# Kernel tuning notes

Measured on AMD Instinct MI355X. Metric: run time of the kernel, lower is better.

The kernel has to match this reference:

```python
import jax, jax.numpy as jnp
import numpy as np

N_NODES = 50000   # batch_size * num_nodes
N_EDGES = 800000
D_IN = 128
D_OUT = 128


def setup_inputs() -> dict:
    key = jax.random.key(0)
    k1, k2, k3, k4 = jax.random.split(key, 4)
    x = jax.random.normal(k1, (N_NODES, D_IN), dtype=jnp.float32)
    edge_index = jax.random.randint(k2, (2, N_EDGES), 0, N_NODES, dtype=jnp.int64)
    W = jax.random.normal(k3, (D_OUT, D_IN), dtype=jnp.float32) * (1.0 / np.sqrt(D_IN))
    b = jax.random.normal(k4, (D_OUT,), dtype=jnp.float32) * 0.01
    return {"x": x, "edge_index": edge_index, "batch_size": 50, "num_nodes": 1000, "W": W, "b": b}


def reference(x, edge_index, batch_size, num_nodes, W, b):
    dim_size = batch_size * num_nodes
    row, col = edge_index[0], edge_index[1]
    # gather messages and segment-mean aggregate over destination rows
    msgs = x[col]                                   # [E, D_IN]
    summed = jax.ops.segment_sum(msgs, row, num_segments=dim_size)      # [N, D_IN]
    counts = jax.ops.segment_sum(jnp.ones((row.shape[0],), dtype=x.dtype), row,
                                 num_segments=dim_size)                 # [N]
    mean = summed / jnp.maximum(counts, 1.0)[:, None]                   # 0 for empty rows
    # linear projection (torch Linear: y = x @ W.T + b)
    return mean @ W.T + b
```

## Files before the change

### kernel.cpp

```cpp
#include <hip/hip_runtime.h>

#define D 128
#define BSHIFT 6
#define BCAP 1536
#define EPB_A 2048

typedef unsigned short ushort_t;
typedef unsigned int uint_t;
typedef __attribute__((ext_vector_type(8))) short short8_t;
typedef __attribute__((ext_vector_type(4))) float f32x4_t;

__device__ __forceinline__ bool eidx_is64(const int* eidx) {
    int lane = threadIdx.x & 63;
    int probe = eidx[2 * lane + 1];
    return __ballot(probe != 0) == 0ULL;
}

__device__ __forceinline__ uint_t f2bf(float f) {
    union { float f; uint_t i; } v; v.f = f;
    return (v.i + 0x7fffu + ((v.i >> 16) & 1u)) >> 16;
}
__device__ __forceinline__ float bf_lo(uint_t w) {
    union { uint_t i; float f; } v; v.i = w << 16; return v.f;
}
__device__ __forceinline__ float bf_hi(uint_t w) {
    union { uint_t i; float f; } v; v.i = w & 0xffff0000u; return v.f;
}

__global__ __launch_bounds__(256) void pre_kernel(
    const int* __restrict__ eidx, int* __restrict__ gcur,
    int* __restrict__ bucket, int E, int NBUK, int ab,
    const float* __restrict__ x, uint_t* __restrict__ xb, int total8, int cvb,
    const float* __restrict__ Wsrc, uint_t* __restrict__ wb, int N) {
    int t = threadIdx.x;

    if ((int)blockIdx.x >= ab) {
        if (xb == nullptr) return;
        int cb = blockIdx.x - ab;
        if (cb < cvb) {
            int i = cb * 256 + t;
            if (i < total8) {
                const float4* p = (const float4*)(x + (size_t)i * 8);
                float4 a = p[0], b = p[1];
                uint4 o;
                o.x = f2bf(a.x) | (f2bf(a.y) << 16);
                o.y = f2bf(a.z) | (f2bf(a.w) << 16);
                o.z = f2bf(b.x) | (f2bf(b.y) << 16);
                o.w = f2bf(b.z) | (f2bf(b.w) << 16);
                *(uint4*)(xb + (size_t)i * 4) = o;
            }
            if (cb == 0 && t < 16) {
                uint4 z; z.x = 0u; z.y = 0u; z.z = 0u; z.w = 0u;
                ((uint4*)(xb + (size_t)N * (D / 2)))[t] = z;
            }
        } else {
            int i = (cb - cvb) * 256 + t;
            if (i < D * D / 8) {
                const float4* p = (const float4*)(Wsrc + (size_t)i * 8);
                float4 a = p[0], b = p[1];
                uint4 o;
                o.x = f2bf(a.x) | (f2bf(a.y) << 16);
                o.y = f2bf(a.z) | (f2bf(a.w) << 16);
                o.z = f2bf(b.x) | (f2bf(b.y) << 16);
                o.w = f2bf(b.z) | (f2bf(b.w) << 16);
                *(uint4*)(wb + (size_t)i * 4) = o;
            }
        }
        return;
    }

    __shared__ int lhist[1024];
    __shared__ int lbase[1024];
    bool is64 = eidx_is64(eidx);
    for (int i = t; i < NBUK; i += 256) lhist[i] = 0;
    __syncthreads();

    int e0 = blockIdx.x * EPB_A;
    int e1 = min(e0 + EPB_A, E);
    int rr[8], cc[8];
    #pragma unroll
    for (int k = 0; k < 8; ++k) {
        int e = e0 + t + k * 256;
        rr[k] = -1;
        if (e < e1) {
            if (is64) { rr[k] = eidx[2 * e]; cc[k] = eidx[2 * E + 2 * e]; }
            else      { rr[k] = eidx[e];     cc[k] = eidx[E + e]; }
            atomicAdd(&lhist[rr[k] >> BSHIFT], 1);
        }
    }
    __syncthreads();
    for (int i = t; i < NBUK; i += 256) {
        int h = lhist[i];
        lbase[i] = (h > 0) ? atomicAdd(&gcur[i], h) : 0;
        lhist[i] = 0;
    }
    __syncthreads();
    #pragma unroll
    for (int k = 0; k < 8; ++k) {
        if (rr[k] >= 0) {
            int b = rr[k] >> BSHIFT;
            int p = atomicAdd(&lhist[b], 1);
            int idx = lbase[b] + p;
            if (idx < BCAP) bucket[b * BCAP + idx] = ((rr[k] & 63) << 24) | cc[k];
        }
    }
}

#define GATHER8(CA, CB)                                                       \
    {                                                                         \
        uint4 g0 = *(const uint4*)(xs + (size_t)(CA).x * D);                  \
        uint4 g1 = *(const uint4*)(xs + (size_t)(CA).y * D);                  \
        uint4 g2 = *(const uint4*)(xs + (size_t)(CA).z * D);                  \
        uint4 g3 = *(const uint4*)(xs + (size_t)(CA).w * D);                  \
        uint4 g4 = *(const uint4*)(xs + (size_t)(CB).x * D);                  \
        uint4 g5 = *(const uint4*)(xs + (size_t)(CB).y * D);                  \
        uint4 g6 = *(const uint4*)(xs + (size_t)(CB).z * D);                  \
        uint4 g7 = *(const uint4*)(xs + (size_t)(CB).w * D);                  \
        a0 += ((bf_lo(g0.x) + bf_lo(g1.x)) + (bf_lo(g2.x) + bf_lo(g3.x)))     \
            + ((bf_lo(g4.x) + bf_lo(g5.x)) + (bf_lo(g6.x) + bf_lo(g7.x)));    \
        a1 += ((bf_hi(g0.x) + bf_hi(g1.x)) + (bf_hi(g2.x) + bf_hi(g3.x)))     \
            + ((bf_hi(g4.x) + bf_hi(g5.x)) + (bf_hi(g6.x) + bf_hi(g7.x)));    \
        a2 += ((bf_lo(g0.y) + bf_lo(g1.y)) + (bf_lo(g2.y) + bf_lo(g3.y)))     \
            + ((bf_lo(g4.y) + bf_lo(g5.y)) + (bf_lo(g6.y) + bf_lo(g7.y)));    \
        a3 += ((bf_hi(g0.y) + bf_hi(g1.y)) + (bf_hi(g2.y) + bf_hi(g3.y)))     \
            + ((bf_hi(g4.y) + bf_hi(g5.y)) + (bf_hi(g6.y) + bf_hi(g7.y)));    \
        a4 += ((bf_lo(g0.z) + bf_lo(g1.z)) + (bf_lo(g2.z) + bf_lo(g3.z)))     \
            + ((bf_lo(g4.z) + bf_lo(g5.z)) + (bf_lo(g6.z) + bf_lo(g7.z)));    \
        a5 += ((bf_hi(g0.z) + bf_hi(g1.z)) + (bf_hi(g2.z) + bf_hi(g3.z)))     \
            + ((bf_hi(g4.z) + bf_hi(g5.z)) + (bf_hi(g6.z) + bf_hi(g7.z)));    \
        a6 += ((bf_lo(g0.w) + bf_lo(g1.w)) + (bf_lo(g2.w) + bf_lo(g3.w)))     \
            + ((bf_lo(g4.w) + bf_lo(g5.w)) + (bf_lo(g6.w) + bf_lo(g7.w)));    \
        a7 += ((bf_hi(g0.w) + bf_hi(g1.w)) + (bf_hi(g2.w) + bf_hi(g3.w)))     \
            + ((bf_hi(g4.w) + bf_hi(g5.w)) + (bf_hi(g6.w) + bf_hi(g7.w)));    \
    }

#define GATHER16(CA, CB, CC, CD)                                              \
    {                                                                         \
        uint4 g0 = *(const uint4*)(xs + (size_t)(CA).x * D);                  \
        uint4 g1 = *(const uint4*)(xs + (size_t)(CA).y * D);                  \
        uint4 g2 = *(const uint4*)(xs + (size_t)(CA).z * D);                  \
        uint4 g3 = *(const uint4*)(xs + (size_t)(CA).w * D);                  \
        uint4 g4 = *(const uint4*)(xs + (size_t)(CB).x * D);                  \
        uint4 g5 = *(const uint4*)(xs + (size_t)(CB).y * D);                  \
        uint4 g6 = *(const uint4*)(xs + (size_t)(CB).z * D);                  \
        uint4 g7 = *(const uint4*)(xs + (size_t)(CB).w * D);                  \
        uint4 g8 = *(const uint4*)(xs + (size_t)(CC).x * D);                  \
        uint4 g9 = *(const uint4*)(xs + (size_t)(CC).y * D);                  \
        uint4 ga = *(const uint4*)(xs + (size_t)(CC).z * D);                  \
        uint4 gb = *(const uint4*)(xs + (size_t)(CC).w * D);                  \
        uint4 gc = *(const uint4*)(xs + (size_t)(CD).x * D);                  \
        uint4 gd = *(const uint4*)(xs + (size_t)(CD).y * D);                  \
        uint4 ge = *(const uint4*)(xs + (size_t)(CD).z * D);                  \
        uint4 gf = *(const uint4*)(xs + (size_t)(CD).w * D);                  \
        a0 += (((bf_lo(g0.x) + bf_lo(g1.x)) + (bf_lo(g2.x) + bf_lo(g3.x)))    \
             + ((bf_lo(g4.x) + bf_lo(g5.x)) + (bf_lo(g6.x) + bf_lo(g7.x))))   \
            + (((bf_lo(g8.x) + bf_lo(g9.x)) + (bf_lo(ga.x) + bf_lo(gb.x)))    \
             + ((bf_lo(gc.x) + bf_lo(gd.x)) + (bf_lo(ge.x) + bf_lo(gf.x))));  \
        a1 += (((bf_hi(g0.x) + bf_hi(g1.x)) + (bf_hi(g2.x) + bf_hi(g3.x)))    \
             + ((bf_hi(g4.x) + bf_hi(g5.x)) + (bf_hi(g6.x) + bf_hi(g7.x))))   \
            + (((bf_hi(g8.x) + bf_hi(g9.x)) + (bf_hi(ga.x) + bf_hi(gb.x)))    \
             + ((bf_hi(gc.x) + bf_hi(gd.x)) + (bf_hi(ge.x) + bf_hi(gf.x))));  \
        a2 += (((bf_lo(g0.y) + bf_lo(g1.y)) + (bf_lo(g2.y) + bf_lo(g3.y)))    \
             + ((bf_lo(g4.y) + bf_lo(g5.y)) + (bf_lo(g6.y) + bf_lo(g7.y))))   \
            + (((bf_lo(g8.y) + bf_lo(g9.y)) + (bf_lo(ga.y) + bf_lo(gb.y)))    \
             + ((bf_lo(gc.y) + bf_lo(gd.y)) + (bf_lo(ge.y) + bf_lo(gf.y))));  \
        a3 += (((bf_hi(g0.y) + bf_hi(g1.y)) + (bf_hi(g2.y) + bf_hi(g3.y)))    \
             + ((bf_hi(g4.y) + bf_hi(g5.y)) + (bf_hi(g6.y) + bf_hi(g7.y))))   \
            + (((bf_hi(g8.y) + bf_hi(g9.y)) + (bf_hi(ga.y) + bf_hi(gb.y)))    \
             + ((bf_hi(gc.y) + bf_hi(gd.y)) + (bf_hi(ge.y) + bf_hi(gf.y))));  \
        a4 += (((bf_lo(g0.z) + bf_lo(g1.z)) + (bf_lo(g2.z) + bf_lo(g3.z)))    \
             + ((bf_lo(g4.z) + bf_lo(g5.z)) + (bf_lo(g6.z) + bf_lo(g7.z))))   \
            + (((bf_lo(g8.z) + bf_lo(g9.z)) + (bf_lo(ga.z) + bf_lo(gb.z)))    \
             + ((bf_lo(gc.z) + bf_lo(gd.z)) + (bf_lo(ge.z) + bf_lo(gf.z))));  \
        a5 += (((bf_hi(g0.z) + bf_hi(g1.z)) + (bf_hi(g2.z) + bf_hi(g3.z)))    \
             + ((bf_hi(g4.z) + bf_hi(g5.z)) + (bf_hi(g6.z) + bf_hi(g7.z))))   \
            + (((bf_hi(g8.z) + bf_hi(g9.z)) + (bf_hi(ga.z) + bf_hi(gb.z)))    \
             + ((bf_hi(gc.z) + bf_hi(gd.z)) + (bf_hi(ge.z) + bf_hi(gf.z))));  \
        a6 += (((bf_lo(g0.w) + bf_lo(g1.w)) + (bf_lo(g2.w) + bf_lo(g3.w)))    \
             + ((bf_lo(g4.w) + bf_lo(g5.w)) + (bf_lo(g6.w) + bf_lo(g7.w))))   \
            + (((bf_lo(g8.w) + bf_lo(g9.w)) + (bf_lo(ga.w) + bf_lo(gb.w)))    \
             + ((bf_lo(gc.w) + bf_lo(gd.w)) + (bf_lo(ge.w) + bf_lo(gf.w))));  \
        a7 += (((bf_hi(g0.w) + bf_hi(g1.w)) + (bf_hi(g2.w) + bf_hi(g3.w)))    \
             + ((bf_hi(g4.w) + bf_hi(g5.w)) + (bf_hi(g6.w) + bf_hi(g7.w))))   \
            + (((bf_hi(g8.w) + bf_hi(g9.w)) + (bf_hi(ga.w) + bf_hi(gb.w)))    \
             + ((bf_hi(gc.w) + bf_hi(gd.w)) + (bf_hi(ge.w) + bf_hi(gf.w))));  \
    }

__global__ __launch_bounds__(512, 2) void fused_bf_kernel(
    const ushort_t* __restrict__ xb, const int* __restrict__ gcur,
    const int* __restrict__ bucket, const ushort_t* __restrict__ Wb,
    const float* __restrict__ bias, float* __restrict__ out, int N) {
    __shared__ int sE[2048];
    __shared__ int lcnt[64], lpos[64], lstart[64];
    __shared__ ushort_t sA[64 * 136];
    int t = threadIdx.x;
    int b = blockIdx.x;

    if (t < 64) { lcnt[t] = 0; lpos[t] = 0; }
    __syncthreads();
    int tot = min(gcur[b], BCAP);
    const int* bp = bucket + (size_t)b * BCAP;
    for (int i = t; i < tot; i += 512)
        atomicAdd(&lcnt[bp[i] >> 24], 1);
    __syncthreads();
    if (t == 0) {
        int run = 0;
        #pragma unroll
        for (int i = 0; i < 64; ++i) {
            lstart[i] = run;
            run += (lcnt[i] + 7) & ~7;
        }
    }
    __syncthreads();
    for (int i = t; i < tot; i += 512) {
        int v = bp[i];
        int rl = v >> 24;
        int p = atomicAdd(&lpos[rl], 1);
        int idx = lstart[rl] + p;
        if (idx < 2048) sE[idx] = v & 0xFFFFFF;
    }
    if (t < 64) {
        int c0 = lcnt[t];
        int pe = (c0 + 7) & ~7;
        for (int p = c0; p < pe; ++p) {
            int idx = lstart[t] + p;
            if (idx < 2048) sE[idx] = N;
        }
    }
    __syncthreads();

    int lane = t & 63, wave = t >> 6;
    int qi = t >> 4, sl = t & 15;
    int nbase = b << BSHIFT;
    const ushort_t* xs = xb + 8 * sl;

    #pragma unroll
    for (int quad = 0; quad < 2; ++quad) {
        int n = 2 * qi + quad;
        int nr  = lcnt[n];
        int st  = lstart[n];
        int nr8 = (nr + 7) & ~7;
        float a0 = 0.f, a1 = 0.f, a2 = 0.f, a3 = 0.f;
        float a4 = 0.f, a5 = 0.f, a6 = 0.f, a7 = 0.f;
        int i = 0;
        for (; i + 16 <= nr8; i += 16) {
            int4 cA = *(const int4*)(sE + st + i);
            int4 cB = *(const int4*)(sE + st + i + 4);
            int4 cC = *(const int4*)(sE + st + i + 8);
            int4 cD = *(const int4*)(sE + st + i + 12);
            GATHER16(cA, cB, cC, cD)
        }
        if (i + 8 <= nr8) {
            int4 dA = *(const int4*)(sE + st + i);
            int4 dB = *(const int4*)(sE + st + i + 4);
            GATHER8(dA, dB)
        }
        float inv = (nr > 0) ? 1.0f / (float)nr : 0.0f;
        uint4 pk;
        pk.x = f2bf(a0 * inv) | (f2bf(a1 * inv) << 16);
        pk.y = f2bf(a2 * inv) | (f2bf(a3 * inv) << 16);
        pk.z = f2bf(a4 * inv) | (f2bf(a5 * inv) << 16);
        pk.w = f2bf(a6 * inv) | (f2bf(a7 * inv) << 16);
        *(uint4*)(sA + n * 136 + 8 * sl) = pk;
    }
    __syncthreads();

    {
        int rt = wave & 3, jgrp = wave >> 2;
        int ml = lane & 15, kh = lane >> 4;
        short8_t afr[4];
        #pragma unroll
        for (int ks = 0; ks < 4; ++ks)
            afr[ks] = *(const short8_t*)(sA + (rt * 16 + ml) * 136 + ks * 32 + kh * 8);
        f32x4_t acc[4];
        #pragma unroll
        for (int q = 0; q < 4; ++q) acc[q] = (f32x4_t){0.f, 0.f, 0.f, 0.f};
        #pragma unroll
        for (int q = 0; q < 4; ++q) {
            int j = (jgrp * 4 + q) * 16 + ml;
            #pragma unroll
            for (int ks = 0; ks < 4; ++ks) {
                short8_t bfr = *(const short8_t*)(Wb + (size_t)j * D + ks * 32 + kh * 8);
                acc[q] = __builtin_amdgcn_mfma_f32_16x16x32_bf16(afr[ks], bfr, acc[q], 0, 0, 0);
            }
        }
        #pragma unroll
        for (int q = 0; q < 4; ++q) {
            int j = (jgrp * 4 + q) * 16 + ml;
            float bj = bias[j];
            #pragma unroll
            for (int r = 0; r < 4; ++r) {
                int gn = nbase + rt * 16 + kh * 4 + r;
                if (gn < N) out[(size_t)gn * D + j] = acc[q][r] + bj;
            }
        }
    }
}

__global__ __launch_bounds__(256) void prep_kernel(
    const int* __restrict__ gcur, const int* __restrict__ bucket,
    int* __restrict__ elist, int* __restrict__ cnt,
    int* __restrict__ start, int N, int NBUK) {
    __shared__ int lcnt[64], lpos[64], lstart[64];
    int t = threadIdx.x;
    int b = blockIdx.x;
    if (t < 64) { lcnt[t] = 0; lpos[t] = 0; }
    __syncthreads();
    int tot = min(gcur[b], BCAP);
    const int* bp = bucket + (size_t)b * BCAP;
    for (int i = t; i < tot; i += 256)
        atomicAdd(&lcnt[bp[i] >> 24], 1);
    __syncthreads();
    if (t == 0) {
        int run = 0;
        #pragma unroll
        for (int i = 0; i < 64; ++i) {
            lstart[i] = run;
            run += (lcnt[i] + 3) & ~3;
        }
    }
    __syncthreads();
    for (int i = t; i < tot; i += 256) {
        int v = bp[i];
        int rl = v >> 24;
        int p = atomicAdd(&lpos[rl], 1);
        int idx = lstart[rl] + p;
        if (idx < BCAP) elist[(size_t)b * BCAP + idx] = v & 0xFFFFFF;
    }
    if (t < 64) {
        int gr = (b << BSHIFT) + t;
        if (gr < N) { cnt[gr] = lcnt[t]; start[gr] = b * BCAP + lstart[t]; }
    }
}

__global__ __launch_bounds__(256, 6) void fused_kernel(
    const float* __restrict__ x, const int* __restrict__ elist,
    const int* __restrict__ cnt, const int* __restrict__ start,
    const float* __restrict__ W, const float* __restrict__ bias,
    float* __restrict__ out, int N) {
    __shared__ float sT[128 * 36];
    __shared__ float wc[16 * 132];
    int t = threadIdx.x;
    int lane = t & 63, wave = t >> 6;
    int half = lane >> 5, sl = lane & 31;
    int nbase = blockIdx.x * 32;

    #pragma unroll
    for (int pair = 0; pair < 4; ++pair) {
        int n = wave * 8 + pair * 2 + half;
        int gn = nbase + n;
        int nr  = (gn < N) ? cnt[gn]   : 0;
        int beg = (gn < N) ? start[gn] : 0;
        int nro  = __shfl(nr, lane ^ 32);
        int both = min(nr, nro);
        float ax = 0.f, ay = 0.f, az = 0.f, aw = 0.f;
        int i = 0;
        for (; i + 8 <= both; i += 8) {
            int4 cA = *(const int4*)(elist + beg + i);
            int4 cB = *(const int4*)(elist + beg + i + 4);
            float4 v0 = *(const float4*)(x + (size_t)cA.x * D + 4 * sl);
            float4 v1 = *(const float4*)(x + (size_t)cA.y * D + 4 * sl);
            float4 v2 = *(const float4*)(x + (size_t)cA.z * D + 4 * sl);
            float4 v3 = *(const float4*)(x + (size_t)cA.w * D + 4 * sl);
            float4 v4 = *(const float4*)(x + (size_t)cB.x * D + 4 * sl);
            float4 v5 = *(const float4*)(x + (size_t)cB.y * D + 4 * sl);
            float4 v6 = *(const float4*)(x + (size_t)cB.z * D + 4 * sl);
            float4 v7 = *(const float4*)(x + (size_t)cB.w * D + 4 * sl);
            ax += ((v0.x + v1.x) + (v2.x + v3.x)) + ((v4.x + v5.x) + (v6.x + v7.x));
            ay += ((v0.y + v1.y) + (v2.y + v3.y)) + ((v4.y + v5.y) + (v6.y + v7.y));
            az += ((v0.z + v1.z) + (v2.z + v3.z)) + ((v4.z + v5.z) + (v6.z + v7.z));
            aw += ((v0.w + v1.w) + (v2.w + v3.w)) + ((v4.w + v5.w) + (v6.w + v7.w));
        }
        for (; i < nr; ++i) {
            int c0 = elist[beg + i];
            float4 v = *(const float4*)(x + (size_t)c0 * D + 4 * sl);
            ax += v.x; ay += v.y; az += v.z; aw += v.w;
        }
        float inv = (nr > 0) ? 1.0f / (float)nr : 0.0f;
        int k0 = 4 * sl;
        sT[(k0 + 0) * 36 + n] = ax * inv;
        sT[(k0 + 1) * 36 + n] = ay * inv;
        sT[(k0 + 2) * 36 + n] = az * inv;
        sT[(k0 + 3) * 36 + n] = aw * inv;
    }

    int jg = t & 31, ng = t >> 5;
    int j0 = jg * 4, n0 = ng * 4;
    float acc[4][4] = {};
    for (int kc = 0; kc < 8; ++kc) {
        __syncthreads();
        #pragma unroll
        for (int i = 0; i < 8; ++i) {
            int idx = t + i * 256;
            int j = idx >> 4, kk = idx & 15;
            wc[kk * 132 + j] = W[j * D + kc * 16 + kk];
        }
        __syncthreads();
        #pragma unroll
        for (int kk = 0; kk < 16; ++kk) {
            int k = kc * 16 + kk;
            float4 s4 = *(const float4*)(sT + k * 36 + n0);
            float4 w4 = *(const float4*)(wc + kk * 132 + j0);
            acc[0][0] = fmaf(s4.x, w4.x, acc[0][0]); acc[0][1] = fmaf(s4.x, w4.y, acc[0][1]);
            acc[0][2] = fmaf(s4.x, w4.z, acc[0][2]); acc[0][3] = fmaf(s4.x, w4.w, acc[0][3]);
            acc[1][0] = fmaf(s4.y, w4.x, acc[1][0]); acc[1][1] = fmaf(s4.y, w4.y, acc[1][1]);
            acc[1][2] = fmaf(s4.y, w4.z, acc[1][2]); acc[1][3] = fmaf(s4.y, w4.w, acc[1][3]);
            acc[2][0] = fmaf(s4.z, w4.x, acc[2][0]); acc[2][1] = fmaf(s4.z, w4.y, acc[2][1]);
            acc[2][2] = fmaf(s4.z, w4.z, acc[2][2]); acc[2][3] = fmaf(s4.z, w4.w, acc[2][3]);
            acc[3][0] = fmaf(s4.w, w4.x, acc[3][0]); acc[3][1] = fmaf(s4.w, w4.y, acc[3][1]);
            acc[3][2] = fmaf(s4.w, w4.z, acc[3][2]); acc[3][3] = fmaf(s4.w, w4.w, acc[3][3]);
        }
    }
    float4 b4 = *(const float4*)(bias + j0);
    #pragma unroll
    for (int i = 0; i < 4; ++i) {
        int gn = nbase + n0 + i;
        if (gn >= N) continue;
        float4 o;
        o.x = acc[i][0] + b4.x;
        o.y = acc[i][1] + b4.y;
        o.z = acc[i][2] + b4.z;
        o.w = acc[i][3] + b4.w;
        *(float4*)(out + (size_t)gn * D + j0) = o;
    }
}

__global__ __launch_bounds__(256) void scatter_kernel(
    const float* __restrict__ x, const int* __restrict__ eidx,
    float* summed, float* __restrict__ counts, int E) {
    int t = blockIdx.x * 256 + threadIdx.x;
    int lane = threadIdx.x & 63;
    bool is64 = eidx_is64(eidx);
    int e = t >> 6;
    if (e >= E) return;
    int d = lane * 2;
    int r, c;
    if (is64) { r = eidx[2 * e]; c = eidx[2 * E + 2 * e]; }
    else      { r = eidx[e];     c = eidx[E + e]; }
    float2 v = *(const float2*)(x + (size_t)c * D + d);
    float* dst = summed + (size_t)r * D + d;
    atomicAdd(dst, v.x);
    atomicAdd(dst + 1, v.y);
    if (lane == 0) atomicAdd(counts + r, 1.0f);
}

__global__ __launch_bounds__(256) void divide_kernel(
    float* __restrict__ sums, const float* __restrict__ counts, int N) {
    int g = blockIdx.x * 256 + threadIdx.x;
    int r = g >> 6, lane = g & 63;
    if (r >= N) return;
    float inv = 1.0f / fmaxf(counts[r], 1.0f);
    float2* p = (float2*)(sums + (size_t)r * D + 2 * lane);
    float2 v = *p;
    v.x *= inv; v.y *= inv;
    *p = v;
}

__global__ __launch_bounds__(256) void gemm_kernel(
    float* inout, const float* __restrict__ W,
    const float* __restrict__ bias, int N) {
    __shared__ float sT[128 * 36];
    __shared__ float wc[32 * 132];
    int t = threadIdx.x;
    int nbase = blockIdx.x * 32;
    #pragma unroll
    for (int i = 0; i < 16; ++i) {
        int idx = t + i * 256;
        int n = idx >> 7, k = idx & 127;
        int gn = nbase + n;
        sT[k * 36 + n] = (gn < N) ? inout[(size_t)gn * D + k] : 0.0f;
    }
    int jg = t & 31, ng = t >> 5;
    int j0 = jg * 4, n0 = ng * 4;
    float acc[4][4] = {};
    for (int kc = 0; kc < 4; ++kc) {
        __syncthreads();
        #pragma unroll
        for (int i = 0; i < 16; ++i) {
            int idx = t + i * 256;
            int j = idx >> 5, kk = idx & 31;
            wc[kk * 132 + j] = W[j * D + kc * 32 + kk];
        }
        __syncthreads();
        #pragma unroll 8
        for (int kk = 0; kk < 32; ++kk) {
            int k = kc * 32 + kk;
            float4 s4 = *(const float4*)(sT + k * 36 + n0);
            float4 w4 = *(const float4*)(wc + kk * 132 + j0);
            acc[0][0] = fmaf(s4.x, w4.x, acc[0][0]); acc[0][1] = fmaf(s4.x, w4.y, acc[0][1]);
            acc[0][2] = fmaf(s4.x, w4.z, acc[0][2]); acc[0][3] = fmaf(s4.x, w4.w, acc[0][3]);
            acc[1][0] = fmaf(s4.y, w4.x, acc[1][0]); acc[1][1] = fmaf(s4.y, w4.y, acc[1][1]);
            acc[1][2] = fmaf(s4.y, w4.z, acc[1][2]); acc[1][3] = fmaf(s4.y, w4.w, acc[1][3]);
            acc[2][0] = fmaf(s4.z, w4.x, acc[2][0]); acc[2][1] = fmaf(s4.z, w4.y, acc[2][1]);
            acc[2][2] = fmaf(s4.z, w4.z, acc[2][2]); acc[2][3] = fmaf(s4.z, w4.w, acc[2][3]);
            acc[3][0] = fmaf(s4.w, w4.x, acc[3][0]); acc[3][1] = fmaf(s4.w, w4.y, acc[3][1]);
            acc[3][2] = fmaf(s4.w, w4.z, acc[3][2]); acc[3][3] = fmaf(s4.w, w4.w, acc[3][3]);
        }
    }
    float4 b4 = *(const float4*)(bias + j0);
    #pragma unroll
    for (int i = 0; i < 4; ++i) {
        int gn = nbase + n0 + i;
        if (gn >= N) continue;
        float4 o;
        o.x = acc[i][0] + b4.x;
        o.y = acc[i][1] + b4.y;
        o.z = acc[i][2] + b4.z;
        o.w = acc[i][3] + b4.w;
        *(float4*)(inout + (size_t)gn * D + j0) = o;
    }
}

extern "C" void kernel_launch(void* const* d_in, const int* in_sizes, int n_in,
                              void* d_out, int out_size, void* d_ws, size_t ws_size,
                              hipStream_t stream) {
    const float* x = (const float*)d_in[0];
    const int* eidx = (const int*)d_in[1];
    const float* W = (const float*)d_in[4];
    const float* b = (const float*)d_in[5];
    float* out = (float*)d_out;

    int N = in_sizes[0] / D;
    int E = in_sizes[1] / 2;
    int NBUK = (N + 63) >> BSHIFT;
    int ab = (E + EPB_A - 1) / EPB_A;

    size_t o0 = 0;
    size_t o_gc = o0;  o0 += ((size_t)NBUK * 4 + 255) & ~255ULL;
    size_t o_cn = o0;  o0 += ((size_t)N * 4 + 255) & ~255ULL;
    size_t o_st = o0;  o0 += ((size_t)N * 4 + 255) & ~255ULL;
    size_t o_bk = o0;  o0 += (size_t)NBUK * BCAP * 4;
    size_t o_el = o0;  o0 += (size_t)NBUK * BCAP * 4;
    size_t base_need = o0;
    size_t o_xb = o0;  o0 += (((size_t)(N + 1) * D * 2) + 255) & ~255ULL;
    size_t o_wb = o0;  size_t bf_need = o0 + (size_t)D * D * 2;

    bool cap_ok = (N <= 65536) && ((size_t)NBUK * BCAP >= (size_t)E);

    int cvb = (N * D / 8 + 255) / 256;
    int wvb = (D * D / 8 + 255) / 256;

    if (cap_ok && ws_size >= bf_need) {
        char* ws = (char*)d_ws;
        int*      gcur  = (int*)(ws + o_gc);
        int*      bkt   = (int*)(ws + o_bk);
        ushort_t* xb    = (ushort_t*)(ws + o_xb);
        ushort_t* wb    = (ushort_t*)(ws + o_wb);

        hipMemsetAsync(gcur, 0, (size_t)NBUK * 4, stream);
        pre_kernel<<<ab + cvb + wvb, 256, 0, stream>>>(
            eidx, gcur, bkt, E, NBUK, ab,
            x, (uint_t*)xb, N * D / 8, cvb, W, (uint_t*)wb, N);
        fused_bf_kernel<<<NBUK, 512, 0, stream>>>(xb, gcur, bkt, wb, b, out, N);
    } else if (cap_ok && ws_size >= base_need) {
        char* ws = (char*)d_ws;
        int* gcur  = (int*)(ws + o_gc);
        int* cnt   = (int*)(ws + o_cn);
        int* start = (int*)(ws + o_st);
        int* bkt   = (int*)(ws + o_bk);
        int* elist = (int*)(ws + o_el);
        int fb = (N + 31) / 32;

        hipMemsetAsync(gcur, 0, (size_t)NBUK * 4, stream);
        pre_kernel<<<ab, 256, 0, stream>>>(
            eidx, gcur, bkt, E, NBUK, ab,
            nullptr, nullptr, 0, 0, nullptr, nullptr, N);
        prep_kernel<<<NBUK, 256, 0, stream>>>(gcur, bkt, elist, cnt, start, N, NBUK);
        fused_kernel<<<fb, 256, 0, stream>>>(x, elist, cnt, start, W, b, out, N);
    } else {
        float* counts = (float*)d_ws;
        int fb = (N + 31) / 32;
        hipMemsetAsync(d_out, 0, (size_t)N * D * sizeof(float), stream);
        hipMemsetAsync(d_ws, 0, (size_t)N * sizeof(float), stream);
        int sb = (E * 64 + 255) / 256;
        scatter_kernel<<<sb, 256, 0, stream>>>(x, eidx, out, counts, E);
        int db = (N * 64 + 255) / 256;
        divide_kernel<<<db, 256, 0, stream>>>(out, counts, N);
        gemm_kernel<<<fb, 256, 0, stream>>>(out, W, b, N);
    }
}
```

Before: 156.9 us.

## Double-buffer neighbor gathers via global_load_lds and shrink buckets to 32 rows

The bf16 gather now uses direct global-to-LDS async loads (global_load_lds) into a per-wave double-buffered staging area, issuing the next four rows before accumulating the current ones, in place of register-based 8/16-wide gathers. Buckets shrink from 64 to 32 destination rows (BCAP 1024), and the fused kernel drops to 256 threads per block, so there are twice as many smaller blocks. The aim is to overlap gather latency with accumulation and raise block-level parallelism. In exchange, each thread has fewer loads in flight, there are more waitcnt stalls, LDS use per block is larger, and the smaller bucket capacity gives less headroom before edges are dropped.

```diff
diff --git a/kernel.cpp b/kernel.cpp
--- a/kernel.cpp
+++ b/kernel.cpp
@@ -1,14 +1,16 @@
 #include <hip/hip_runtime.h>
 
 #define D 128
-#define BSHIFT 6
-#define BCAP 1536
+#define BSHIFT 5
+#define BCAP 1024
 #define EPB_A 2048
 
 typedef unsigned short ushort_t;
 typedef unsigned int uint_t;
 typedef __attribute__((ext_vector_type(8))) short short8_t;
 typedef __attribute__((ext_vector_type(4))) float f32x4_t;
+typedef const __attribute__((address_space(1))) void* gas_cptr;
+typedef __attribute__((address_space(3))) void* las_ptr;
 
 __device__ __forceinline__ bool eidx_is64(const int* eidx) {
     int lane = threadIdx.x & 63;
@@ -69,8 +71,8 @@
         return;
     }
 
-    __shared__ int lhist[1024];
-    __shared__ int lbase[1024];
+    __shared__ int lhist[2048];
+    __shared__ int lbase[2048];
     bool is64 = eidx_is64(eidx);
     for (int i = t; i < NBUK; i += 256) lhist[i] = 0;
     __syncthreads();
@@ -101,130 +103,74 @@
             int b = rr[k] >> BSHIFT;
             int p = atomicAdd(&lhist[b], 1);
             int idx = lbase[b] + p;
-            if (idx < BCAP) bucket[b * BCAP + idx] = ((rr[k] & 63) << 24) | cc[k];
-        }
-    }
-}
-
-#define GATHER8(CA, CB)                                                       \
+            if (idx < BCAP) bucket[b * BCAP + idx] = ((rr[k] & 31) << 24) | cc[k];
+        }
+    }
+}
+
+#define ISSUE(c, bufsel)                                                      \
     {                                                                         \
-        uint4 g0 = *(const uint4*)(xs + (size_t)(CA).x * D);                  \
-        uint4 g1 = *(const uint4*)(xs + (size_t)(CA).y * D);                  \
-        uint4 g2 = *(const uint4*)(xs + (size_t)(CA).z * D);                  \
-        uint4 g3 = *(const uint4*)(xs + (size_t)(CA).w * D);                  \
-        uint4 g4 = *(const uint4*)(xs + (size_t)(CB).x * D);                  \
-        uint4 g5 = *(const uint4*)(xs + (size_t)(CB).y * D);                  \
-        uint4 g6 = *(const uint4*)(xs + (size_t)(CB).z * D);                  \
-        uint4 g7 = *(const uint4*)(xs + (size_t)(CB).w * D);                  \
-        a0 += ((bf_lo(g0.x) + bf_lo(g1.x)) + (bf_lo(g2.x) + bf_lo(g3.x)))     \
-            + ((bf_lo(g4.x) + bf_lo(g5.x)) + (bf_lo(g6.x) + bf_lo(g7.x)));    \
-        a1 += ((bf_hi(g0.x) + bf_hi(g1.x)) + (bf_hi(g2.x) + bf_hi(g3.x)))     \
-            + ((bf_hi(g4.x) + bf_hi(g5.x)) + (bf_hi(g6.x) + bf_hi(g7.x)));    \
-        a2 += ((bf_lo(g0.y) + bf_lo(g1.y)) + (bf_lo(g2.y) + bf_lo(g3.y)))     \
-            + ((bf_lo(g4.y) + bf_lo(g5.y)) + (bf_lo(g6.y) + bf_lo(g7.y)));    \
-        a3 += ((bf_hi(g0.y) + bf_hi(g1.y)) + (bf_hi(g2.y) + bf_hi(g3.y)))     \
-            + ((bf_hi(g4.y) + bf_hi(g5.y)) + (bf_hi(g6.y) + bf_hi(g7.y)));    \
-        a4 += ((bf_lo(g0.z) + bf_lo(g1.z)) + (bf_lo(g2.z) + bf_lo(g3.z)))     \
-            + ((bf_lo(g4.z) + bf_lo(g5.z)) + (bf_lo(g6.z) + bf_lo(g7.z)));    \
-        a5 += ((bf_hi(g0.z) + bf_hi(g1.z)) + (bf_hi(g2.z) + bf_hi(g3.z)))     \
-            + ((bf_hi(g4.z) + bf_hi(g5.z)) + (bf_hi(g6.z) + bf_hi(g7.z)));    \
-        a6 += ((bf_lo(g0.w) + bf_lo(g1.w)) + (bf_lo(g2.w) + bf_lo(g3.w)))     \
-            + ((bf_lo(g4.w) + bf_lo(g5.w)) + (bf_lo(g6.w) + bf_lo(g7.w)));    \
-        a7 += ((bf_hi(g0.w) + bf_hi(g1.w)) + (bf_hi(g2.w) + bf_hi(g3.w)))     \
-            + ((bf_hi(g4.w) + bf_hi(g5.w)) + (bf_hi(g6.w) + bf_hi(g7.w)));    \
-    }
-
-#define GATHER16(CA, CB, CC, CD)                                              \
-    {                                                                         \
-        uint4 g0 = *(const uint4*)(xs + (size_t)(CA).x * D);                  \
-        uint4 g1 = *(const uint4*)(xs + (size_t)(CA).y * D);                  \
-        uint4 g2 = *(const uint4*)(xs + (size_t)(CA).z * D);                  \
-        uint4 g3 = *(const uint4*)(xs + (size_t)(CA).w * D);                  \
-        uint4 g4 = *(const uint4*)(xs + (size_t)(CB).x * D);                  \
-        uint4 g5 = *(const uint4*)(xs + (size_t)(CB).y * D);                  \
-        uint4 g6 = *(const uint4*)(xs + (size_t)(CB).z * D);                  \
-        uint4 g7 = *(const uint4*)(xs + (size_t)(CB).w * D);                  \
-        uint4 g8 = *(const uint4*)(xs + (size_t)(CC).x * D);                  \
-        uint4 g9 = *(const uint4*)(xs + (size_t)(CC).y * D);                  \
-        uint4 ga = *(const uint4*)(xs + (size_t)(CC).z * D);                  \
-        uint4 gb = *(const uint4*)(xs + (size_t)(CC).w * D);                  \
-        uint4 gc = *(const uint4*)(xs + (size_t)(CD).x * D);                  \
-        uint4 gd = *(const uint4*)(xs + (size_t)(CD).y * D);                  \
-        uint4 ge = *(const uint4*)(xs + (size_t)(CD).z * D);                  \
-        uint4 gf = *(const uint4*)(xs + (size_t)(CD).w * D);                  \
-        a0 += (((bf_lo(g0.x) + bf_lo(g1.x)) + (bf_lo(g2.x) + bf_lo(g3.x)))    \
-             + ((bf_lo(g4.x) + bf_lo(g5.x)) + (bf_lo(g6.x) + bf_lo(g7.x))))   \
-            + (((bf_lo(g8.x) + bf_lo(g9.x)) + (bf_lo(ga.x) + bf_lo(gb.x)))    \
-             + ((bf_lo(gc.x) + bf_lo(gd.x)) + (bf_lo(ge.x) + bf_lo(gf.x))));  \
-        a1 += (((bf_hi(g0.x) + bf_hi(g1.x)) + (bf_hi(g2.x) + bf_hi(g3.x)))    \
-             + ((bf_hi(g4.x) + bf_hi(g5.x)) + (bf_hi(g6.x) + bf_hi(g7.x))))   \
-            + (((bf_hi(g8.x) + bf_hi(g9.x)) + (bf_hi(ga.x) + bf_hi(gb.x)))    \
-             + ((bf_hi(gc.x) + bf_hi(gd.x)) + (bf_hi(ge.x) + bf_hi(gf.x))));  \
-        a2 += (((bf_lo(g0.y) + bf_lo(g1.y)) + (bf_lo(g2.y) + bf_lo(g3.y)))    \
-             + ((bf_lo(g4.y) + bf_lo(g5.y)) + (bf_lo(g6.y) + bf_lo(g7.y))))   \
-            + (((bf_lo(g8.y) + bf_lo(g9.y)) + (bf_lo(ga.y) + bf_lo(gb.y)))    \
-             + ((bf_lo(gc.y) + bf_lo(gd.y)) + (bf_lo(ge.y) + bf_lo(gf.y))));  \
-        a3 += (((bf_hi(g0.y) + bf_hi(g1.y)) + (bf_hi(g2.y) + bf_hi(g3.y)))    \
-             + ((bf_hi(g4.y) + bf_hi(g5.y)) + (bf_hi(g6.y) + bf_hi(g7.y))))   \
-            + (((bf_hi(g8.y) + bf_hi(g9.y)) + (bf_hi(ga.y) + bf_hi(gb.y)))    \
-             + ((bf_hi(gc.y) + bf_hi(gd.y)) + (bf_hi(ge.y) + bf_hi(gf.y))));  \
-        a4 += (((bf_lo(g0.z) + bf_lo(g1.z)) + (bf_lo(g2.z) + bf_lo(g3.z)))    \
-             + ((bf_lo(g4.z) + bf_lo(g5.z)) + (bf_lo(g6.z) + bf_lo(g7.z))))   \
-            + (((bf_lo(g8.z) + bf_lo(g9.z)) + (bf_lo(ga.z) + bf_lo(gb.z)))    \
-             + ((bf_lo(gc.z) + bf_lo(gd.z)) + (bf_lo(ge.z) + bf_lo(gf.z))));  \
-        a5 += (((bf_hi(g0.z) + bf_hi(g1.z)) + (bf_hi(g2.z) + bf_hi(g3.z)))    \
-             + ((bf_hi(g4.z) + bf_hi(g5.z)) + (bf_hi(g6.z) + bf_hi(g7.z))))   \
-            + (((bf_hi(g8.z) + bf_hi(g9.z)) + (bf_hi(ga.z) + bf_hi(gb.z)))    \
-             + ((bf_hi(gc.z) + bf_hi(gd.z)) + (bf_hi(ge.z) + bf_hi(gf.z))));  \
-        a6 += (((bf_lo(g0.w) + bf_lo(g1.w)) + (bf_lo(g2.w) + bf_lo(g3.w)))    \
-             + ((bf_lo(g4.w) + bf_lo(g5.w)) + (bf_lo(g6.w) + bf_lo(g7.w))))   \
-            + (((bf_lo(g8.w) + bf_lo(g9.w)) + (bf_lo(ga.w) + bf_lo(gb.w)))    \
-             + ((bf_lo(gc.w) + bf_lo(gd.w)) + (bf_lo(ge.w) + bf_lo(gf.w))));  \
-        a7 += (((bf_hi(g0.w) + bf_hi(g1.w)) + (bf_hi(g2.w) + bf_hi(g3.w)))    \
-             + ((bf_hi(g4.w) + bf_hi(g5.w)) + (bf_hi(g6.w) + bf_hi(g7.w))))   \
-            + (((bf_hi(g8.w) + bf_hi(g9.w)) + (bf_hi(ga.w) + bf_hi(gb.w)))    \
-             + ((bf_hi(gc.w) + bf_hi(gd.w)) + (bf_hi(ge.w) + bf_hi(gf.w))));  \
-    }
-
-__global__ __launch_bounds__(512, 2) void fused_bf_kernel(
+        ushort_t* db_ = wstage + (bufsel) * 2048;                             \
+        __builtin_amdgcn_global_load_lds(                                     \
+            (gas_cptr)(xb + (size_t)(c).x * D + 8 * sl),                      \
+            (las_ptr)(db_), 16, 0, 0);                                        \
+        __builtin_amdgcn_global_load_lds(                                     \
+            (gas_cptr)(xb + (size_t)(c).y * D + 8 * sl),                      \
+            (las_ptr)(db_ + 512), 16, 0, 0);                                  \
+        __builtin_amdgcn_global_load_lds(                                     \
+            (gas_cptr)(xb + (size_t)(c).z * D + 8 * sl),                      \
+            (las_ptr)(db_ + 1024), 16, 0, 0);                                 \
+        __builtin_amdgcn_global_load_lds(                                     \
+            (gas_cptr)(xb + (size_t)(c).w * D + 8 * sl),                      \
+            (las_ptr)(db_ + 1536), 16, 0, 0);                                 \
+    }
+
+#define ACC(v)                                                                \
+    a0 += bf_lo((v).x); a1 += bf_hi((v).x);                                   \
+    a2 += bf_lo((v).y); a3 += bf_hi((v).y);                                   \
+    a4 += bf_lo((v).z); a5 += bf_hi((v).z);                                   \
+    a6 += bf_lo((v).w); a7 += bf_hi((v).w);
+
+__global__ __launch_bounds__(256, 3) void fused_bf_kernel(
     const ushort_t* __restrict__ xb, const int* __restrict__ gcur,
     const int* __restrict__ bucket, const ushort_t* __restrict__ Wb,
     const float* __restrict__ bias, float* __restrict__ out, int N) {
-    __shared__ int sE[2048];
-    __shared__ int lcnt[64], lpos[64], lstart[64];
-    __shared__ ushort_t sA[64 * 136];
+    __shared__ int sE[1024];
+    __shared__ int lcnt[32], lpos[32], lstart[32];
+    __shared__ ushort_t sA[32 * 136];
+    __shared__ ushort_t stage[16384];
     int t = threadIdx.x;
     int b = blockIdx.x;
 
-    if (t < 64) { lcnt[t] = 0; lpos[t] = 0; }
+    if (t < 32) { lcnt[t] = 0; lpos[t] = 0; }
     __syncthreads();
     int tot = min(gcur[b], BCAP);
     const int* bp = bucket + (size_t)b * BCAP;
-    for (int i = t; i < tot; i += 512)
+    for (int i = t; i < tot; i += 256)
         atomicAdd(&lcnt[bp[i] >> 24], 1);
     __syncthreads();
     if (t == 0) {
         int run = 0;
         #pragma unroll
-        for (int i = 0; i < 64; ++i) {
+        for (int i = 0; i < 32; ++i) {
             lstart[i] = run;
             run += (lcnt[i] + 7) & ~7;
         }
     }
     __syncthreads();
-    for (int i = t; i < tot; i += 512) {
+    for (int i = t; i < tot; i += 256) {
         int v = bp[i];
         int rl = v >> 24;
         int p = atomicAdd(&lpos[rl], 1);
         int idx = lstart[rl] + p;
-        if (idx < 2048) sE[idx] = v & 0xFFFFFF;
-    }
-    if (t < 64) {
+        if (idx < 1024) sE[idx] = v & 0xFFFFFF;
+    }
+    if (t < 32) {
         int c0 = lcnt[t];
         int pe = (c0 + 7) & ~7;
         for (int p = c0; p < pe; ++p) {
             int idx = lstart[t] + p;
-            if (idx < 2048) sE[idx] = N;
+            if (idx < 1024) sE[idx] = N;
         }
     }
     __syncthreads();
@@ -232,28 +178,42 @@
     int lane = t & 63, wave = t >> 6;
     int qi = t >> 4, sl = t & 15;
     int nbase = b << BSHIFT;
-    const ushort_t* xs = xb + 8 * sl;
+    ushort_t* wstage = stage + (wave << 12);
 
     #pragma unroll
     for (int quad = 0; quad < 2; ++quad) {
         int n = 2 * qi + quad;
-        int nr  = lcnt[n];
-        int st  = lstart[n];
-        int nr8 = (nr + 7) & ~7;
+        int nr = lcnt[n];
+        int st = lstart[n];
+        int trips = ((nr + 7) & ~7) >> 2;
+        int wmax = trips;
+        wmax = max(wmax, __shfl_xor(wmax, 16));
+        wmax = max(wmax, __shfl_xor(wmax, 32));
         float a0 = 0.f, a1 = 0.f, a2 = 0.f, a3 = 0.f;
         float a4 = 0.f, a5 = 0.f, a6 = 0.f, a7 = 0.f;
-        int i = 0;
-        for (; i + 16 <= nr8; i += 16) {
-            int4 cA = *(const int4*)(sE + st + i);
-            int4 cB = *(const int4*)(sE + st + i + 4);
-            int4 cC = *(const int4*)(sE + st + i + 8);
-            int4 cD = *(const int4*)(sE + st + i + 12);
-            GATHER16(cA, cB, cC, cD)
-        }
-        if (i + 8 <= nr8) {
-            int4 dA = *(const int4*)(sE + st + i);
-            int4 dB = *(const int4*)(sE + st + i + 4);
-            GATHER8(dA, dB)
+        if (wmax > 0) {
+            int4 c0 = (0 < trips) ? *(const int4*)(sE + st)
+                                  : make_int4(N, N, N, N);
+            ISSUE(c0, 0)
+            for (int bt = 0; bt < wmax; ++bt) {
+                int buf = bt & 1;
+                if (bt + 1 < wmax) {
+                    int4 cn = (bt + 1 < trips)
+                        ? *(const int4*)(sE + st + 4 * (bt + 1))
+                        : make_int4(N, N, N, N);
+                    ISSUE(cn, buf ^ 1)
+                    asm volatile("s_waitcnt vmcnt(4)" ::: "memory");
+                } else {
+                    asm volatile("s_waitcnt vmcnt(0)" ::: "memory");
+                }
+                __builtin_amdgcn_sched_barrier(0);
+                const ushort_t* sb = wstage + buf * 2048;
+                uint4 v0 = *(const uint4*)(sb +    0 + lane * 8);
+                uint4 v1 = *(const uint4*)(sb +  512 + lane * 8);
+                uint4 v2 = *(const uint4*)(sb + 1024 + lane * 8);
+                uint4 v3 = *(const uint4*)(sb + 1536 + lane * 8);
+                ACC(v0) ACC(v1) ACC(v2) ACC(v3)
+            }
         }
         float inv = (nr > 0) ? 1.0f / (float)nr : 0.0f;
         uint4 pk;
@@ -266,7 +226,7 @@
     __syncthreads();
 
     {
-        int rt = wave & 3, jgrp = wave >> 2;
+        int rt = wave & 1, jgrp = wave >> 1;
         int ml = lane & 15, kh = lane >> 4;
         short8_t afr[4];
         #pragma unroll
@@ -301,10 +261,10 @@
     const int* __restrict__ gcur, const int* __restrict__ bucket,
     int* __restrict__ elist, int* __restrict__ cnt,
     int* __restrict__ start, int N, int NBUK) {
-    __shared__ int lcnt[64], lpos[64], lstart[64];
+    __shared__ int lcnt[32], lpos[32], lstart[32];
     int t = threadIdx.x;
     int b = blockIdx.x;
-    if (t < 64) { lcnt[t] = 0; lpos[t] = 0; }
+    if (t < 32) { lcnt[t] = 0; lpos[t] = 0; }
     __syncthreads();
     int tot = min(gcur[b], BCAP);
     const int* bp = bucket + (size_t)b * BCAP;
@@ -314,7 +274,7 @@
     if (t == 0) {
         int run = 0;
         #pragma unroll
-        for (int i = 0; i < 64; ++i) {
+        for (int i = 0; i < 32; ++i) {
             lstart[i] = run;
             run += (lcnt[i] + 3) & ~3;
         }
@@ -327,7 +287,7 @@
         int idx = lstart[rl] + p;
         if (idx < BCAP) elist[(size_t)b * BCAP + idx] = v & 0xFFFFFF;
     }
-    if (t < 64) {
+    if (t < 32) {
         int gr = (b << BSHIFT) + t;
         if (gr < N) { cnt[gr] = lcnt[t]; start[gr] = b * BCAP + lstart[t]; }
     }
@@ -522,7 +482,7 @@
 
     int N = in_sizes[0] / D;
     int E = in_sizes[1] / 2;
-    int NBUK = (N + 63) >> BSHIFT;
+    int NBUK = (N + 31) >> BSHIFT;
     int ab = (E + EPB_A - 1) / EPB_A;
 
     size_t o0 = 0;
@@ -551,7 +511,7 @@
         pre_kernel<<<ab + cvb + wvb, 256, 0, stream>>>(
             eidx, gcur, bkt, E, NBUK, ab,
             x, (uint_t*)xb, N * D / 8, cvb, W, (uint_t*)wb, N);
-        fused_bf_kernel<<<NBUK, 512, 0, stream>>>(xb, gcur, bkt, wb, b, out, N);
+        fused_bf_kernel<<<NBUK, 256, 0, stream>>>(xb, gcur, bkt, wb, b, out, N);
     } else if (cap_ok && ws_size >= base_need) {
         char* ws = (char*)d_ws;
         int* gcur  = (int*)(ws + o_gc);
```

After: 164.0 us. 4.6% more time.
